# Kernel optimization log

Measured on AMD Instinct MI355X. Metric: run time of the kernel, lower is better.

Reference implementation:

```python
import jax, jax.numpy as jnp
import numpy as np

BS, SL, INDIM, D, H = 2, 2048, 1024, 64, 16
DH = D * H


def _rotation_buffers(sl, units):
    # int rotation_values branch: values=arange(sl), min_lam=1, max_lam=1000
    half = units // 2
    min_lam, max_lam = 1.0, 1000.0
    theta = min_lam / (2.0 * np.pi) * (max_lam / min_lam) ** (2.0 * np.arange(half) / units)
    pos = np.arange(sl, dtype=np.float64)[:, None] / theta[None]  # [sl, half]
    # tile([...,2]).reshape == repeat each entry twice along last dim -> [sl, units]
    rcos = np.repeat(np.cos(pos), 2, axis=-1).astype(np.float32)
    rsin = np.repeat(np.sin(pos), 2, axis=-1).astype(np.float32)
    return jnp.asarray(rcos), jnp.asarray(rsin)


def setup_inputs() -> dict:
    key = jax.random.key(0)
    ks = jax.random.split(key, 8)
    s = 0.02
    x = jax.random.normal(ks[0], (BS, SL, INDIM), jnp.float32)
    mask = jnp.zeros((BS, SL), jnp.float32)  # subtracted from logits; zeros = no masking
    Wqkv = jax.random.normal(ks[1], (INDIM, 3 * DH), jnp.float32) * s
    bqkv = jnp.zeros((3 * DH,), jnp.float32)
    Wo = jax.random.normal(ks[2], (DH, INDIM), jnp.float32) * s
    bo = jnp.zeros((INDIM,), jnp.float32)
    Wg = jax.random.normal(ks[3], (INDIM, DH), jnp.float32) * s
    bg = jnp.zeros((DH,), jnp.float32)
    Wb = jax.random.normal(ks[4], (INDIM, H), jnp.float32) * s
    bb = jnp.zeros((H,), jnp.float32)
    alphaq = jnp.zeros((), jnp.float32)
    alphak = jnp.zeros((), jnp.float32)
    alphav = jnp.zeros((), jnp.float32)
    rcos, rsin = _rotation_buffers(SL, D)
    return dict(x=x, mask=mask, Wqkv=Wqkv, bqkv=bqkv, Wo=Wo, bo=bo, Wg=Wg, bg=bg,
                Wb=Wb, bb=bb, alphaq=alphaq, alphak=alphak, alphav=alphav,
                rcos=rcos, rsin=rsin)


def _rotate(X, cos, sin_even):
    # Faithful to the in-place torch code:
    #   X_ = X*cos; X_[...,::2] += -sin[...,::2]*X_[...,1::2];
    #   X_[...,1::2] += sin[...,::2]*X_[...,::2]   (uses UPDATED even lanes)
    Xc = X * cos
    even = Xc[..., 0::2] - sin_even * Xc[..., 1::2]
    odd = Xc[..., 1::2] + sin_even * even
    return jnp.stack([even, odd], axis=-1).reshape(X.shape)


def reference(x, mask, Wqkv, bqkv, Wo, bo, Wg, bg, Wb, bb, alphaq, alphak, alphav, rcos, rsin):
    bs, sl, _ = x.shape
    qkv = x @ Wqkv + bqkv  # [bs, sl, 3*DH]
    Q, K, V = jnp.split(qkv, 3, axis=-1)
    # split last dim as (d, h) and move heads out: [bs, h, sl, d]
    def split_heads(t):
        return t.reshape(bs, sl, D, H).transpose(0, 3, 1, 2)
    Q = split_heads(Q) * jax.nn.sigmoid(alphaq)
    K = split_heads(K) * jax.nn.sigmoid(alphak)
    V = split_heads(V) * jax.nn.sigmoid(alphav)
    cos = rcos[:sl]            # [sl, d]
    sin_even = rsin[:sl, 0::2]  # [sl, d/2]
    Q = _rotate(Q, cos, sin_even)
    K = _rotate(K, cos, sin_even)
    scale = D ** (-0.5)
    QK = scale * jnp.einsum('bhqd,bhkd->bhqk', Q, K)  # [bs,h,sl,sl]
    # 'regular' bias: Wb(x) -> [bs,sl,h] -> [bs,h,1,sl] broadcast over queries
    B = (x @ Wb + bb)
    QK = QK + jnp.transpose(B, (0, 2, 1))[:, :, None, :]
    QK = QK - mask[:, None, None, :]
    w = jax.nn.softmax(QK, axis=-1)
    att = jnp.einsum('bhqk,bhkd->bhqd', w, V)  # [bs,h,sl,d]
    # sigmoid gate, split the same (d,h) way
    G = jax.nn.sigmoid(x @ Wg + bg).reshape(bs, sl, D, H).transpose(0, 3, 1, 2)
    att = att * G
    # merge heads back as (d, h) -> [bs, sl, d*h]
    att = att.transpose(0, 2, 3, 1).reshape(bs, sl, DH)
    resid = att @ Wo + bo
    return x + resid  # identity shortcut (out_units == indim), dropout=0
```

## Files before the change

kernel.cpp:

```cpp
#include <hip/hip_runtime.h>
#include <cstdint>

typedef unsigned short u16;
typedef unsigned int   u32;
typedef __bf16 bf16x8 __attribute__((ext_vector_type(8)));
typedef u16    u16x8  __attribute__((ext_vector_type(8)));
typedef float  f32x4  __attribute__((ext_vector_type(4)));
typedef float  f32x16 __attribute__((ext_vector_type(16)));
typedef u32    u32x2v __attribute__((ext_vector_type(2)));
typedef __attribute__((address_space(3))) void lds_void;
typedef __attribute__((address_space(1))) void gl_void;

#define GLDS16(gsrc, ldst) \
  __builtin_amdgcn_global_load_lds((gl_void*)(gsrc), (lds_void*)(ldst), 16, 0, 0)

#define DEV __device__ __forceinline__
#define LOG2E 1.4426950408889634f

#if defined(__has_builtin)
#if __has_builtin(__builtin_amdgcn_exp2f)
#define EXP2(x) __builtin_amdgcn_exp2f(x)
#endif
#endif
#ifndef EXP2
#define EXP2(x) exp2f(x)
#endif

DEV u16 f2bf(float f) {
  uint32_t u = __float_as_uint(f);
  u += 0x7fff + ((u >> 16) & 1);
  return (u16)(u >> 16);
}
DEV float bf2f(u16 h) { return __uint_as_float(((uint32_t)h) << 16); }
DEV float sigm(float x) { return 1.0f / (1.0f + __expf(-x)); }

__global__ __launch_bounds__(256) void cvtx_k(const float* __restrict__ x, u16* __restrict__ xb) {
  int i = blockIdx.x * 256 + threadIdx.x;
  float4 v = ((const float4*)x)[i];
  ushort4 o;
  o.x = f2bf(v.x); o.y = f2bf(v.y); o.z = f2bf(v.z); o.w = f2bf(v.w);
  ((ushort4*)xb)[i] = o;
}

template <int PERM>
__global__ __launch_bounds__(256) void wtransp_k(const float* __restrict__ W, u16* __restrict__ Wt,
                                                 int K, int N) {
  __shared__ float tile[32][33];
  int kt = blockIdx.x, nt = blockIdx.y;
  int t = threadIdx.x;
  int r = t >> 5, c = t & 31;
#pragma unroll
  for (int i = 0; i < 4; ++i)
    tile[r + i * 8][c] = W[(size_t)(kt * 32 + r + i * 8) * N + nt * 32 + c];
  __syncthreads();
#pragma unroll
  for (int i = 0; i < 4; ++i) {
    int ko = kt * 32 + c;
    int kdst = PERM ? ((ko & 15) * 64 + (ko >> 4)) : ko;
    Wt[(size_t)(nt * 32 + r + i * 8) * K + kdst] = f2bf(tile[c][r + i * 8]);
  }
}

__global__ __launch_bounds__(64) void biasb_k(const float* __restrict__ x, const float* __restrict__ Wb,
                                              const float* __restrict__ bb, const float* __restrict__ mask,
                                              float* __restrict__ bmT) {
  int row = blockIdx.x;
  int l = threadIdx.x;
  const float* xr = x + (size_t)row * 1024;
  float acc[16];
#pragma unroll
  for (int h = 0; h < 16; ++h) acc[h] = 0.f;
  for (int it = 0; it < 16; ++it) {
    int k = l + it * 64;
    float xv = xr[k];
    const float4* wr = (const float4*)(Wb + k * 16);
#pragma unroll
    for (int q = 0; q < 4; ++q) {
      float4 wv = wr[q];
      acc[q * 4 + 0] += xv * wv.x; acc[q * 4 + 1] += xv * wv.y;
      acc[q * 4 + 2] += xv * wv.z; acc[q * 4 + 3] += xv * wv.w;
    }
  }
#pragma unroll
  for (int h = 0; h < 16; ++h) {
    float v = acc[h];
#pragma unroll
    for (int m = 32; m >= 1; m >>= 1) v += __shfl_xor(v, m, 64);
    acc[h] = v;
  }
  if (l < 16) {
    int b = row >> 11, s = row & 2047;
    bmT[(size_t)(b * 16 + l) * 2048 + s] = (acc[l] + bb[l] - mask[row]) * LOG2E;
  }
}

__global__ __launch_bounds__(256) void gemmF_k(const u16* __restrict__ A, const u16* __restrict__ Bt,
                                               const float* __restrict__ bqkv, const float* __restrict__ bg,
                                               u16* __restrict__ qkvb, u16* __restrict__ gh_rm) {
  __shared__ u16 sAB[4][4096];
  const int t = threadIdx.x, w = t >> 6, l = t & 63;
  const int lr = l & 15, lg = l >> 4;
  const int bm = blockIdx.x, bn = blockIdx.y;
  const int wr = w >> 1, wc = w & 1;
  f32x4 acc[4][4] = {};

  auto stage = [&](int buf, int kt) {
    u16* As = sAB[buf * 2];
    u16* Bs = sAB[buf * 2 + 1];
#pragma unroll
    for (int r = 0; r < 2; ++r) {
      int L = r * 256 + t;
      GLDS16(A + (size_t)(bm * 128 + (L >> 2)) * 1024 + (kt * 32 + (L & 3) * 8),
             &As[(r * 256 + w * 64) * 8]);
      GLDS16(Bt + (size_t)(bn * 128 + (L >> 2)) * 1024 + (kt * 32 + (L & 3) * 8),
             &Bs[(r * 256 + w * 64) * 8]);
    }
  };

  stage(0, 0);
  __syncthreads();
  for (int kt = 0; kt < 32; ++kt) {
    int buf = kt & 1;
    if (kt < 31) stage(buf ^ 1, kt + 1);
    const u16* As = sAB[buf * 2];
    const u16* Bs = sAB[buf * 2 + 1];
    bf16x8 af[4], bfr[4];
#pragma unroll
    for (int m = 0; m < 4; ++m) af[m] = *(const bf16x8*)&As[(wr * 64 + m * 16 + lr) * 32 + lg * 8];
#pragma unroll
    for (int n = 0; n < 4; ++n) bfr[n] = *(const bf16x8*)&Bs[(wc * 64 + n * 16 + lr) * 32 + lg * 8];
#pragma unroll
    for (int m = 0; m < 4; ++m)
#pragma unroll
      for (int n = 0; n < 4; ++n)
        acc[m][n] = __builtin_amdgcn_mfma_f32_16x16x32_bf16(af[m], bfr[n], acc[m][n], 0, 0, 0);
    __syncthreads();
  }
#pragma unroll
  for (int m = 0; m < 4; ++m)
#pragma unroll
    for (int n = 0; n < 4; ++n) {
      int col = bn * 128 + wc * 64 + n * 16 + lr;
      float bv = (bn < 24) ? bqkv[col] : bg[col - 3072];
#pragma unroll
      for (int rg = 0; rg < 4; ++rg) {
        int row = bm * 128 + wr * 64 + m * 16 + lg * 4 + rg;
        float v = acc[m][n][rg] + bv;
        if (bn < 24) qkvb[(size_t)row * 3072 + col] = f2bf(v);
        else         gh_rm[(size_t)row * 1024 + (col - 3072)] = f2bf(sigm(v));
      }
    }
}

__global__ __launch_bounds__(256) void relayout_k(const u16* __restrict__ qkv,
    const u16* __restrict__ gh_rm,
    const float* __restrict__ rcos, const float* __restrict__ rsin,
    const float* __restrict__ aq, const float* __restrict__ ak, const float* __restrict__ av,
    u16* __restrict__ Qh, u16* __restrict__ Kh, u16* __restrict__ Vh, u16* __restrict__ Gh) {
  int row = blockIdx.x;
  int b = row >> 11, s = row & 2047;
  int t = threadIdx.x;
  float sq = sigm(*aq) * 0.125f * LOG2E, sk = sigm(*ak), sv = sigm(*av);
  const u16* qrow = qkv + (size_t)row * 3072;
  if (t < 128) {
    int which = t >> 6;
    int idx = t & 63;
    int hoct = idx & 1, dp = idx >> 1;
    const u16* src = qrow + which * 1024;
    float sc = which ? sk : sq;
    u16* dst = which ? Kh : Qh;
    float cc = rcos[s * 64 + 2 * dp];
    float sn = rsin[s * 64 + 2 * dp];
    u16x8 Av = *(const u16x8*)(src + dp * 32 + hoct * 8);
    u16x8 Bv = *(const u16x8*)(src + dp * 32 + 16 + hoct * 8);
#pragma unroll
    for (int j = 0; j < 8; ++j) {
      float xe = bf2f(Av[j]) * sc, xo = bf2f(Bv[j]) * sc;
      float e = cc * xe - sn * (cc * xo);
      float o2 = cc * xo + sn * e;
      u32 pk = (u32)f2bf(e) | ((u32)f2bf(o2) << 16);
      *(u32*)&dst[((size_t)(b * 16 + hoct * 8 + j) * 2048 + s) * 64 + 2 * dp] = pk;
    }
  }
  {
    const u16* src = qrow + 2048;
    int h = t >> 4, d0 = (t & 15) * 4;
    ushort4 o4;
    o4.x = f2bf(bf2f(src[(d0 + 0) * 16 + h]) * sv);
    o4.y = f2bf(bf2f(src[(d0 + 1) * 16 + h]) * sv);
    o4.z = f2bf(bf2f(src[(d0 + 2) * 16 + h]) * sv);
    o4.w = f2bf(bf2f(src[(d0 + 3) * 16 + h]) * sv);
    *(ushort4*)&Vh[((size_t)(b * 16 + h) * 2048 + s) * 64 + d0] = o4;
  }
  {
    const u16* src = gh_rm + (size_t)row * 1024;
    int h = t >> 4, d0 = (t & 15) * 4;
    ushort4 o4;
    o4.x = src[(d0 + 0) * 16 + h];
    o4.y = src[(d0 + 1) * 16 + h];
    o4.z = src[(d0 + 2) * 16 + h];
    o4.w = src[(d0 + 3) * 16 + h];
    *(ushort4*)&Gh[((size_t)(b * 16 + h) * 2048 + s) * 64 + d0] = o4;
  }
}

__global__ __launch_bounds__(256) void vtrans_k(const u16* __restrict__ Vh, u16* __restrict__ VTg) {
  __shared__ u16 vt[4096];
  int bh = blockIdx.x, kt = blockIdx.y;
  int t = threadIdx.x;
  {
    int kp = t >> 3, dc = t & 7;
    const u16* vsrc = Vh + ((size_t)bh * 2048 + kt * 64 + kp * 2) * 64 + dc * 8;
    u16x8 v0 = *(const u16x8*)vsrc;
    u16x8 v1 = *(const u16x8*)(vsrc + 64);
#pragma unroll
    for (int j = 0; j < 8; ++j) {
      int d = dc * 8 + j;
      int sw = (d & 7) ^ ((d >> 3) & 7);
      *(u32*)((char*)vt + d * 128 + ((kp * 4) ^ (sw << 4))) = (u32)v0[j] | ((u32)v1[j] << 16);
    }
  }
  __syncthreads();
  {
    int d = t >> 2, ch = t & 3;
    int sw = (d & 7) ^ ((d >> 3) & 7);
    u16x8 a = *(const u16x8*)((const char*)vt + d * 128 + ((ch ^ sw) << 4));
    u16x8 b = *(const u16x8*)((const char*)vt + d * 128 + (((ch + 4) ^ sw) << 4));
    u16* dst = VTg + ((size_t)bh * 64 + d) * 2048 + kt * 64;
    *(u16x8*)(dst + ch * 8) = a;
    *(u16x8*)(dst + (ch + 4) * 8) = b;
  }
}

__global__ __launch_bounds__(256) void attn4_k(const u16* __restrict__ Qh, const u16* __restrict__ Kh,
    const u16* __restrict__ VTg, const float* __restrict__ bmT, const u16* __restrict__ Gh,
    u16* __restrict__ attg2) {
  __shared__ u16 smem[16384];
  const int t = threadIdx.x, w = t >> 6, l = t & 63;
  const int q32 = l & 31, hi = l >> 5;
  const int bid = blockIdx.x;
  const int xcd = bid & 7, within = bid >> 3;
  const int bh = xcd * 4 + (within & 3);
  const int qt = within >> 2;
  const int q0w = qt * 128 + w * 32;

  bf16x8 qf[4];
  {
    const u16* qbase = Qh + ((size_t)bh * 2048 + q0w + q32) * 64 + hi * 8;
#pragma unroll
    for (int ks = 0; ks < 4; ++ks) qf[ks] = *(const bf16x8*)(qbase + ks * 16);
  }
  f32x16 o0 = {}, o1 = {};
  float mi = -1e30f, li = 0.f;

  auto stage = [&](int buf, int kt) {
    u16* KsT = smem + buf * 8192;
    u16* VTsT = KsT + 4096;
#pragma unroll
    for (int r = 0; r < 2; ++r) {
      int L = r * 256 + t;
      int row = L >> 3, kc = L & 7;
      GLDS16(Kh + ((size_t)bh * 2048 + kt * 64 + row) * 64 + ((kc ^ (row & 7)) * 8),
             &KsT[(r * 256 + w * 64) * 8]);
    }
#pragma unroll
    for (int r = 0; r < 2; ++r) {
      int L = r * 256 + t;
      int d = L >> 3, kc = L & 7;
      GLDS16(VTg + ((size_t)bh * 64 + d) * 2048 + kt * 64 + ((kc ^ (d & 7)) * 8),
             &VTsT[(r * 256 + w * 64) * 8]);
    }
  };

  stage(0, 0);
  __syncthreads();

  for (int kt = 0; kt < 32; ++kt) {
    int buf = kt & 1;
    if (kt < 31) stage(buf ^ 1, kt + 1);
    const u16* Ks = smem + buf * 8192;
    const u16* VTs = Ks + 4096;
    float bv0 = bmT[(size_t)bh * 2048 + kt * 64 + q32];
    float bv1 = bmT[(size_t)bh * 2048 + kt * 64 + 32 + q32];
#pragma unroll
    for (int sub = 0; sub < 2; ++sub) {
      f32x16 s = {};
#pragma unroll
      for (int ks = 0; ks < 4; ++ks) {
        bf16x8 kf = *(const bf16x8*)((const char*)Ks + (sub * 32 + q32) * 128 +
                                     (((2 * ks + hi) ^ (q32 & 7)) << 4));
        s = __builtin_amdgcn_mfma_f32_32x32x16_bf16(kf, qf[ks], s, 0, 0, 0);
      }
      {
        float bvs = sub ? bv1 : bv0;
        u32 bvb;
        asm("v_cvt_pk_bf16_f32 %0, %1, %2" : "=v"(bvb) : "v"(bvs), "v"(0.f));
        union { u32 wd[4]; bf16x8 v; } Ab = {}, Bb = {};
        Ab.wd[0] = hi ? 0u : bvb;
        Bb.wd[0] = hi ? 0u : 0x3F80u;
        s = __builtin_amdgcn_mfma_f32_32x32x16_bf16(Ab.v, Bb.v, s, 0, 0, 0);
      }
      float tm = fmaxf(fmaxf(s[0], s[1]), s[2]);
      tm = fmaxf(fmaxf(tm, s[3]), s[4]);
      tm = fmaxf(fmaxf(tm, s[5]), s[6]);
      tm = fmaxf(fmaxf(tm, s[7]), s[8]);
      tm = fmaxf(fmaxf(tm, s[9]), s[10]);
      tm = fmaxf(fmaxf(tm, s[11]), s[12]);
      tm = fmaxf(fmaxf(tm, s[13]), s[14]);
      tm = fmaxf(tm, s[15]);
      tm = fmaxf(tm, __shfl_xor(tm, 32, 64));
      if (!__all(tm <= mi + 8.f)) {
        float mn = fmaxf(mi, tm);
        float fac = EXP2(mi - mn);
        mi = mn; li *= fac;
#pragma unroll
        for (int r = 0; r < 16; ++r) { o0[r] *= fac; o1[r] *= fac; }
      }
      float p[16];
#pragma unroll
      for (int r = 0; r < 16; ++r) p[r] = EXP2(s[r] - mi);
      float s0 = (p[0] + p[1]) + (p[2] + p[3]);
      float s1 = (p[4] + p[5]) + (p[6] + p[7]);
      float s2 = (p[8] + p[9]) + (p[10] + p[11]);
      float s3 = (p[12] + p[13]) + (p[14] + p[15]);
      li += (s0 + s1) + (s2 + s3);
      u32 c[8];
#pragma unroll
      for (int i2 = 0; i2 < 8; ++i2)
        asm("v_cvt_pk_bf16_f32 %0, %1, %2" : "=v"(c[i2]) : "v"(p[2 * i2]), "v"(p[2 * i2 + 1]));
      asm volatile("v_permlane32_swap_b32 %0, %1" : "+v"(c[0]), "+v"(c[2]));
      asm volatile("v_permlane32_swap_b32 %0, %1" : "+v"(c[1]), "+v"(c[3]));
      asm volatile("v_permlane32_swap_b32 %0, %1" : "+v"(c[4]), "+v"(c[6]));
      asm volatile("v_permlane32_swap_b32 %0, %1" : "+v"(c[5]), "+v"(c[7]));
      union { u32 wd[4]; bf16x8 v; } pf0, pf1;
      pf0.wd[0] = c[0]; pf0.wd[1] = c[1]; pf0.wd[2] = c[2]; pf0.wd[3] = c[3];
      pf1.wd[0] = c[4]; pf1.wd[1] = c[5]; pf1.wd[2] = c[6]; pf1.wd[3] = c[7];
#pragma unroll
      for (int ks2 = 0; ks2 < 2; ++ks2) {
        int chunk = sub * 4 + ks2 * 2 + hi;
        const bf16x8* pv = ks2 ? &pf1.v : &pf0.v;
        {
          int d = q32;
          bf16x8 vf = *(const bf16x8*)((const char*)VTs + d * 128 + ((chunk ^ (d & 7)) << 4));
          o0 = __builtin_amdgcn_mfma_f32_32x32x16_bf16(vf, *pv, o0, 0, 0, 0);
        }
        {
          int d = 32 + q32;
          bf16x8 vf = *(const bf16x8*)((const char*)VTs + d * 128 + ((chunk ^ (d & 7)) << 4));
          o1 = __builtin_amdgcn_mfma_f32_32x32x16_bf16(vf, *pv, o1, 0, 0, 0);
        }
      }
    }
    __syncthreads();
  }
  li += __shfl_xor(li, 32, 64);
  float inv = 1.f / li;
#pragma unroll
  for (int r = 0; r < 16; ++r) { o0[r] *= inv; o1[r] *= inv; }
  {
    char* ob = (char*)smem + w * 4096;
#pragma unroll
    for (int dt = 0; dt < 2; ++dt) {
#pragma unroll
      for (int rq = 0; rq < 4; ++rq) {
        int dbase = rq * 8 + hi * 4 + dt * 32;
        float e0v = dt ? o1[rq * 4 + 0] : o0[rq * 4 + 0];
        float e1v = dt ? o1[rq * 4 + 1] : o0[rq * 4 + 1];
        float e2v = dt ? o1[rq * 4 + 2] : o0[rq * 4 + 2];
        float e3v = dt ? o1[rq * 4 + 3] : o0[rq * 4 + 3];
        u32 lo = (u32)f2bf(e0v) | ((u32)f2bf(e1v) << 16);
        u32 h2 = (u32)f2bf(e2v) | ((u32)f2bf(e3v) << 16);
        u32x2v val = {lo, h2};
        *(u32x2v*)(ob + q32 * 128 + ((dbase * 2) ^ ((q32 & 7) << 4))) = val;
      }
    }
    const u16* gbase = Gh + ((size_t)bh * 2048 + q0w) * 64;
    u16* abase = attg2 + ((size_t)bh * 2048 + q0w) * 64;
#pragma unroll
    for (int cc = 0; cc < 4; ++cc) {
      int off16 = cc * 64 + l;
      int q = off16 >> 3;
      int inner = (off16 & 7) << 4;
      u16x8 ov = *(const u16x8*)(ob + q * 128 + (inner ^ ((q & 7) << 4)));
      u16x8 gv = *(const u16x8*)(gbase + off16 * 8);
      u16x8 outv;
#pragma unroll
      for (int jj = 0; jj < 8; ++jj) outv[jj] = f2bf(bf2f(ov[jj]) * bf2f(gv[jj]));
      *(u16x8*)(abase + off16 * 8) = outv;
    }
  }
}

__global__ __launch_bounds__(256) void gemm2_k(const u16* __restrict__ A, const u16* __restrict__ Bt,
                                               const float* __restrict__ bo, const float* __restrict__ x,
                                               float* __restrict__ out) {
  __shared__ u16 sA[2][2048];
  __shared__ u16 sB[2][4096];
  const int t = threadIdx.x, w = t >> 6, l = t & 63;
  const int lr = l & 15, lg = l >> 4;
  const int bm = blockIdx.x, bn = blockIdx.y;
  const int wr = w >> 1, wc = w & 1;
  f32x4 acc[2][4] = {};

  auto stage = [&](int buf, int kt) {
    {
      int arow = bm * 64 + (t >> 2), ak = kt * 32 + (t & 3) * 8;
      size_t aoff = ((size_t)((arow >> 11) * 16 + (ak >> 6)) * 2048 + (arow & 2047)) * 64 + (ak & 63);
      GLDS16(A + aoff, &sA[buf][w * 64 * 8]);
    }
#pragma unroll
    for (int r = 0; r < 2; ++r) {
      int L = r * 256 + t;
      GLDS16(Bt + (size_t)(bn * 128 + (L >> 2)) * 1024 + (kt * 32 + (L & 3) * 8),
             &sB[buf][(r * 256 + w * 64) * 8]);
    }
  };

  stage(0, 0);
  __syncthreads();
  for (int kt = 0; kt < 32; ++kt) {
    int buf = kt & 1;
    if (kt < 31) stage(buf ^ 1, kt + 1);
    bf16x8 af[2], bfr[4];
#pragma unroll
    for (int m = 0; m < 2; ++m) af[m] = *(const bf16x8*)&sA[buf][(wr * 32 + m * 16 + lr) * 32 + lg * 8];
#pragma unroll
    for (int n = 0; n < 4; ++n) bfr[n] = *(const bf16x8*)&sB[buf][(wc * 64 + n * 16 + lr) * 32 + lg * 8];
#pragma unroll
    for (int m = 0; m < 2; ++m)
#pragma unroll
      for (int n = 0; n < 4; ++n)
        acc[m][n] = __builtin_amdgcn_mfma_f32_16x16x32_bf16(af[m], bfr[n], acc[m][n], 0, 0, 0);
    __syncthreads();
  }
#pragma unroll
  for (int m = 0; m < 2; ++m)
#pragma unroll
    for (int n = 0; n < 4; ++n) {
      int col = bn * 128 + wc * 64 + n * 16 + lr;
      float bv = bo[col];
#pragma unroll
      for (int rg = 0; rg < 4; ++rg) {
        int row = bm * 64 + wr * 32 + m * 16 + lg * 4 + rg;
        out[(size_t)row * 1024 + col] = acc[m][n][rg] + bv + x[(size_t)row * 1024 + col];
      }
    }
}

extern "C" void kernel_launch(void* const* d_in, const int* in_sizes, int n_in,
                              void* d_out, int out_size, void* d_ws, size_t ws_size,
                              hipStream_t stream) {
  (void)in_sizes; (void)n_in; (void)out_size; (void)ws_size;
  const float* x    = (const float*)d_in[0];
  const float* mask = (const float*)d_in[1];
  const float* Wqkv = (const float*)d_in[2];
  const float* bqkv = (const float*)d_in[3];
  const float* Wo   = (const float*)d_in[4];
  const float* bo   = (const float*)d_in[5];
  const float* Wg   = (const float*)d_in[6];
  const float* bg   = (const float*)d_in[7];
  const float* Wb   = (const float*)d_in[8];
  const float* bb   = (const float*)d_in[9];
  const float* aq   = (const float*)d_in[10];
  const float* ak   = (const float*)d_in[11];
  const float* av   = (const float*)d_in[12];
  const float* rcos = (const float*)d_in[13];
  const float* rsin = (const float*)d_in[14];
  float* out = (float*)d_out;

  char* ws = (char*)d_ws;
  size_t o = 0;
  u16* x_bf   = (u16*)(ws + o); o += (size_t)4096 * 1024 * 2;
  u16* wcat   = (u16*)(ws + o); o += (size_t)4096 * 1024 * 2;
  u16* wo_t2  = (u16*)(ws + o); o += (size_t)1024 * 1024 * 2;
  u16* qkv_b  = (u16*)(ws + o); o += (size_t)4096 * 3072 * 2;
  u16* gh_rm  = (u16*)(ws + o); o += (size_t)4096 * 1024 * 2;
  u16* Gh     = (u16*)(ws + o); o += (size_t)32 * 2048 * 64 * 2;
  u16* Qh     = (u16*)(ws + o); o += (size_t)32 * 2048 * 64 * 2;
  u16* Kh     = (u16*)(ws + o); o += (size_t)32 * 2048 * 64 * 2;
  u16* Vh     = (u16*)(ws + o); o += (size_t)32 * 2048 * 64 * 2;
  u16* VTg    = (u16*)(ws + o); o += (size_t)32 * 64 * 2048 * 2;
  float* bmT  = (float*)(ws + o); o += (size_t)32 * 2048 * 4;
  u16* attg2  = Vh;

  cvtx_k<<<4096, 256, 0, stream>>>(x, x_bf);
  wtransp_k<0><<<dim3(32, 96), 256, 0, stream>>>(Wqkv, wcat, 1024, 3072);
  wtransp_k<0><<<dim3(32, 32), 256, 0, stream>>>(Wg, wcat + (size_t)3072 * 1024, 1024, 1024);
  wtransp_k<1><<<dim3(32, 32), 256, 0, stream>>>(Wo, wo_t2, 1024, 1024);
  biasb_k<<<4096, 64, 0, stream>>>(x, Wb, bb, mask, bmT);
  gemmF_k<<<dim3(32, 32), 256, 0, stream>>>(x_bf, wcat, bqkv, bg, qkv_b, gh_rm);
  relayout_k<<<4096, 256, 0, stream>>>(qkv_b, gh_rm, rcos, rsin, aq, ak, av, Qh, Kh, Vh, Gh);
  vtrans_k<<<dim3(32, 32), 256, 0, stream>>>(Vh, VTg);
  attn4_k<<<512, 256, 0, stream>>>(Qh, Kh, VTg, bmT, Gh, attg2);
  gemm2_k<<<dim3(64, 8), 256, 0, stream>>>(attg2, wo_t2, bo, x, out);
}
```

Measured before the change: 299.2 us.

## Use 4-stage LDS ring with one barrier per step in GEMMs and attention

Replaces the double-buffered LDS pipeline in the QKV GEMM, the attention kernel and the output GEMM with a 4-slot ring that prefetches two tiles ahead. Each step uses a partial vmcnt wait and a single s_barrier instead of two __syncthreads. The attention kernel also prefetches the key-bias values two tiles ahead in registers. Doubling the LDS footprint may lower occupancy. Because kt wraps with &31, the last iterations issue redundant loads into slots that are never read. The exp2 builtin macro is dropped in favour of plain exp2f.

```diff
diff --git a/kernel.cpp b/kernel.cpp
--- a/kernel.cpp
+++ b/kernel.cpp
@@ -17,15 +17,6 @@
 #define DEV __device__ __forceinline__
 #define LOG2E 1.4426950408889634f
 
-#if defined(__has_builtin)
-#if __has_builtin(__builtin_amdgcn_exp2f)
-#define EXP2(x) __builtin_amdgcn_exp2f(x)
-#endif
-#endif
-#ifndef EXP2
-#define EXP2(x) exp2f(x)
-#endif
-
 DEV u16 f2bf(float f) {
   uint32_t u = __float_as_uint(f);
   u += 0x7fff + ((u >> 16) & 1);
@@ -97,7 +88,7 @@
 __global__ __launch_bounds__(256) void gemmF_k(const u16* __restrict__ A, const u16* __restrict__ Bt,
                                                const float* __restrict__ bqkv, const float* __restrict__ bg,
                                                u16* __restrict__ qkvb, u16* __restrict__ gh_rm) {
-  __shared__ u16 sAB[4][4096];
+  __shared__ u16 sAB[4][2][4096];
   const int t = threadIdx.x, w = t >> 6, l = t & 63;
   const int lr = l & 15, lg = l >> 4;
   const int bm = blockIdx.x, bn = blockIdx.y;
@@ -105,8 +96,9 @@
   f32x4 acc[4][4] = {};
 
   auto stage = [&](int buf, int kt) {
-    u16* As = sAB[buf * 2];
-    u16* Bs = sAB[buf * 2 + 1];
+    kt &= 31;
+    u16* As = &sAB[buf][0][0];
+    u16* Bs = &sAB[buf][1][0];
 #pragma unroll
     for (int r = 0; r < 2; ++r) {
       int L = r * 256 + t;
@@ -118,12 +110,16 @@
   };
 
   stage(0, 0);
-  __syncthreads();
+  stage(1, 1);
+#pragma unroll 4
   for (int kt = 0; kt < 32; ++kt) {
-    int buf = kt & 1;
-    if (kt < 31) stage(buf ^ 1, kt + 1);
-    const u16* As = sAB[buf * 2];
-    const u16* Bs = sAB[buf * 2 + 1];
+    const int buf = kt & 3;
+    stage((kt + 2) & 3, kt + 2);
+    asm volatile("s_waitcnt vmcnt(8)" ::: "memory");
+    __builtin_amdgcn_s_barrier();
+    __builtin_amdgcn_sched_barrier(0);
+    const u16* As = &sAB[buf][0][0];
+    const u16* Bs = &sAB[buf][1][0];
     bf16x8 af[4], bfr[4];
 #pragma unroll
     for (int m = 0; m < 4; ++m) af[m] = *(const bf16x8*)&As[(wr * 64 + m * 16 + lr) * 32 + lg * 8];
@@ -134,8 +130,8 @@
 #pragma unroll
       for (int n = 0; n < 4; ++n)
         acc[m][n] = __builtin_amdgcn_mfma_f32_16x16x32_bf16(af[m], bfr[n], acc[m][n], 0, 0, 0);
-    __syncthreads();
-  }
+  }
+  asm volatile("s_waitcnt vmcnt(0)" ::: "memory");
 #pragma unroll
   for (int m = 0; m < 4; ++m)
 #pragma unroll
@@ -232,10 +228,10 @@
   }
 }
 
-__global__ __launch_bounds__(256) void attn4_k(const u16* __restrict__ Qh, const u16* __restrict__ Kh,
+__global__ __launch_bounds__(256) void attn5_k(const u16* __restrict__ Qh, const u16* __restrict__ Kh,
     const u16* __restrict__ VTg, const float* __restrict__ bmT, const u16* __restrict__ Gh,
     u16* __restrict__ attg2) {
-  __shared__ u16 smem[16384];
+  __shared__ u16 smem[32768];
   const int t = threadIdx.x, w = t >> 6, l = t & 63;
   const int q32 = l & 31, hi = l >> 5;
   const int bid = blockIdx.x;
@@ -254,6 +250,7 @@
   float mi = -1e30f, li = 0.f;
 
   auto stage = [&](int buf, int kt) {
+    kt &= 31;
     u16* KsT = smem + buf * 8192;
     u16* VTsT = KsT + 4096;
 #pragma unroll
@@ -272,16 +269,27 @@
     }
   };
 
+  const float* bmb = bmT + (size_t)bh * 2048;
+  float bvA[2], bvB[2];
   stage(0, 0);
-  __syncthreads();
-
+  bvA[0] = bmb[q32];       bvB[0] = bmb[32 + q32];
+  stage(1, 1);
+  bvA[1] = bmb[64 + q32];  bvB[1] = bmb[96 + q32];
+
+#pragma unroll 4
   for (int kt = 0; kt < 32; ++kt) {
-    int buf = kt & 1;
-    if (kt < 31) stage(buf ^ 1, kt + 1);
+    const int buf = kt & 3;
+    stage((kt + 2) & 3, kt + 2);
+    int nk = (kt + 2) & 31;
+    float nb0 = bmb[nk * 64 + q32];
+    float nb1 = bmb[nk * 64 + 32 + q32];
+    float bv0 = bvA[kt & 1], bv1 = bvB[kt & 1];
+    bvA[kt & 1] = nb0; bvB[kt & 1] = nb1;
+    asm volatile("s_waitcnt vmcnt(12)" ::: "memory");
+    __builtin_amdgcn_s_barrier();
+    __builtin_amdgcn_sched_barrier(0);
     const u16* Ks = smem + buf * 8192;
     const u16* VTs = Ks + 4096;
-    float bv0 = bmT[(size_t)bh * 2048 + kt * 64 + q32];
-    float bv1 = bmT[(size_t)bh * 2048 + kt * 64 + 32 + q32];
 #pragma unroll
     for (int sub = 0; sub < 2; ++sub) {
       f32x16 s = {};
@@ -311,14 +319,14 @@
       tm = fmaxf(tm, __shfl_xor(tm, 32, 64));
       if (!__all(tm <= mi + 8.f)) {
         float mn = fmaxf(mi, tm);
-        float fac = EXP2(mi - mn);
+        float fac = exp2f(mi - mn);
         mi = mn; li *= fac;
 #pragma unroll
         for (int r = 0; r < 16; ++r) { o0[r] *= fac; o1[r] *= fac; }
       }
       float p[16];
 #pragma unroll
-      for (int r = 0; r < 16; ++r) p[r] = EXP2(s[r] - mi);
+      for (int r = 0; r < 16; ++r) p[r] = exp2f(s[r] - mi);
       float s0 = (p[0] + p[1]) + (p[2] + p[3]);
       float s1 = (p[4] + p[5]) + (p[6] + p[7]);
       float s2 = (p[8] + p[9]) + (p[10] + p[11]);
@@ -351,8 +359,10 @@
         }
       }
     }
-    __syncthreads();
-  }
+  }
+  asm volatile("s_waitcnt vmcnt(0)" ::: "memory");
+  __builtin_amdgcn_s_barrier();
+
   li += __shfl_xor(li, 32, 64);
   float inv = 1.f / li;
 #pragma unroll
@@ -394,8 +404,8 @@
 __global__ __launch_bounds__(256) void gemm2_k(const u16* __restrict__ A, const u16* __restrict__ Bt,
                                                const float* __restrict__ bo, const float* __restrict__ x,
                                                float* __restrict__ out) {
-  __shared__ u16 sA[2][2048];
-  __shared__ u16 sB[2][4096];
+  __shared__ u16 sA[4][2048];
+  __shared__ u16 sB[4][4096];
   const int t = threadIdx.x, w = t >> 6, l = t & 63;
   const int lr = l & 15, lg = l >> 4;
   const int bm = blockIdx.x, bn = blockIdx.y;
@@ -403,6 +413,7 @@
   f32x4 acc[2][4] = {};
 
   auto stage = [&](int buf, int kt) {
+    kt &= 31;
     {
       int arow = bm * 64 + (t >> 2), ak = kt * 32 + (t & 3) * 8;
       size_t aoff = ((size_t)((arow >> 11) * 16 + (ak >> 6)) * 2048 + (arow & 2047)) * 64 + (ak & 63);
@@ -417,10 +428,14 @@
   };
 
   stage(0, 0);
-  __syncthreads();
+  stage(1, 1);
+#pragma unroll 4
   for (int kt = 0; kt < 32; ++kt) {
-    int buf = kt & 1;
-    if (kt < 31) stage(buf ^ 1, kt + 1);
+    const int buf = kt & 3;
+    stage((kt + 2) & 3, kt + 2);
+    asm volatile("s_waitcnt vmcnt(6)" ::: "memory");
+    __builtin_amdgcn_s_barrier();
+    __builtin_amdgcn_sched_barrier(0);
     bf16x8 af[2], bfr[4];
 #pragma unroll
     for (int m = 0; m < 2; ++m) af[m] = *(const bf16x8*)&sA[buf][(wr * 32 + m * 16 + lr) * 32 + lg * 8];
@@ -431,8 +446,8 @@
 #pragma unroll
       for (int n = 0; n < 4; ++n)
         acc[m][n] = __builtin_amdgcn_mfma_f32_16x16x32_bf16(af[m], bfr[n], acc[m][n], 0, 0, 0);
-    __syncthreads();
-  }
+  }
+  asm volatile("s_waitcnt vmcnt(0)" ::: "memory");
 #pragma unroll
   for (int m = 0; m < 2; ++m)
 #pragma unroll
@@ -491,6 +506,6 @@
   gemmF_k<<<dim3(32, 32), 256, 0, stream>>>(x_bf, wcat, bqkv, bg, qkv_b, gh_rm);
   relayout_k<<<4096, 256, 0, stream>>>(qkv_b, gh_rm, rcos, rsin, aq, ak, av, Qh, Kh, Vh, Gh);
   vtrans_k<<<dim3(32, 32), 256, 0, stream>>>(Vh, VTg);
-  attn4_k<<<512, 256, 0, stream>>>(Qh, Kh, VTg, bmT, Gh, attg2);
+  attn5_k<<<512, 256, 0, stream>>>(Qh, Kh, VTg, bmT, Gh, attg2);
   gemm2_k<<<dim3(64, 8), 256, 0, stream>>>(attg2, wo_t2, bo, x, out);
 }
```

Result: no change. 302.2 us (+1.0%).
